# Optimization experiments

Measured on AMD Instinct MI355X. Metric: run time of the kernel, lower is better.

The kernel has to match this reference:

```python
import jax, jax.numpy as jnp
import numpy as np

DIM = 512
HEADS = 8
HEAD_DIM = DIM // HEADS // 2  # 32
KS = 7  # kernel_size
DIL = 1


def _window_and_pb_start(length, ks):
    nh = ks // 2
    i = jnp.arange(length)
    ni = jnp.clip(i - nh, 0, length - ks)                       # neighborhood start
    pi = nh + jnp.maximum(nh - i, 0) + jnp.where(i + nh >= length, length - i - 1 - nh, 0)
    return ni, pi


def na_attention(qkv_na, rpb):
    # qkv_na: [B,H,W,3*heads*hd]
    B, H, W, _ = qkv_na.shape
    qkv = qkv_na.reshape(B, H, W, 3, HEADS, HEAD_DIM)
    qkv = jnp.transpose(qkv, (3, 0, 4, 1, 2, 5))                 # [3,B,h,H,W,d]
    q, k, v = qkv[0], qkv[1], qkv[2]
    scale = HEAD_DIM ** -0.5
    ni, pi = _window_and_pb_start(H, KS)
    nj, pj = _window_and_pb_start(W, KS)
    off = jnp.arange(KS)
    idx_i = ni[:, None] + off[None, :]                           # [H,K]
    idx_j = nj[:, None] + off[None, :]                           # [W,K]
    # gather neighborhoods: [B,h,H,W,K,K,d]
    kn = k[:, :, idx_i[:, None, :, None], idx_j[None, :, None, :], :]
    vn = v[:, :, idx_i[:, None, :, None], idx_j[None, :, None, :], :]
    bias_i = pi[:, None] + off[None, :]                          # [H,K]
    bias_j = pj[:, None] + off[None, :]                          # [W,K]
    bias = rpb[:, bias_i[:, None, :, None], bias_j[None, :, None, :]]  # [h,H,W,K,K]
    attn = jnp.einsum('bhijd,bhijkld->bhijkl', q * scale, kn) + bias[None]
    a = attn.reshape(B, HEADS, H, W, KS * KS)
    a = jax.nn.softmax(a, axis=-1).reshape(B, HEADS, H, W, KS, KS)
    out = jnp.einsum('bhijkl,bhijkld->bhijd', a, vn)             # [B,h,H,W,d]
    return jnp.transpose(out, (0, 2, 3, 1, 4)).reshape(B, H, W, HEADS * HEAD_DIM)


def self_attention(qkv_self):
    # qkv_self: [B,H,W,3*heads*hd]
    B, H, W, _ = qkv_self.shape
    N = H * W
    qkv = qkv_self.reshape(B, N, 3, HEADS, HEAD_DIM)
    qkv = jnp.transpose(qkv, (2, 0, 3, 1, 4))                    # [3,B,h,N,d]
    q, k, v = qkv[0], qkv[1], qkv[2]
    scale = HEAD_DIM ** -0.5
    scores = jnp.einsum('bhnd,bhmd->bhnm', q * scale, k)
    a = jax.nn.softmax(scores, axis=-1)
    out = jnp.einsum('bhnm,bhmd->bhnd', a, v)
    out = jnp.transpose(out, (0, 2, 1, 3)).reshape(B, H, W, HEADS * HEAD_DIM)
    return out


def setup_inputs() -> dict:
    key = jax.random.key(0)
    ks = jax.random.split(key, 6)
    B, H, W = 2, 48, 48
    x = jax.random.normal(ks[0], (B, H, W, DIM), dtype=jnp.float32)
    W_qkv = jax.random.normal(ks[1], (DIM, 3 * DIM), dtype=jnp.float32) * (DIM ** -0.5)
    b_qkv = jax.random.normal(ks[2], (3 * DIM,), dtype=jnp.float32) * 0.02
    rpb = jax.random.normal(ks[3], (HEADS, 2 * KS - 1, 2 * KS - 1), dtype=jnp.float32) * 0.02
    W_proj = jax.random.normal(ks[4], (DIM, DIM), dtype=jnp.float32) * (DIM ** -0.5)
    b_proj = jax.random.normal(ks[5], (DIM,), dtype=jnp.float32) * 0.02
    return {"x": x, "W_qkv": W_qkv, "b_qkv": b_qkv, "rpb": rpb, "W_proj": W_proj, "b_proj": b_proj}


def reference(x, W_qkv, b_qkv, rpb, W_proj, b_proj):
    B, H, W, C = x.shape
    qkv = x @ W_qkv + b_qkv                                      # [B,H,W,3C]
    qkv_na, qkv_self = qkv[..., : 3 * C // 2], qkv[..., 3 * C // 2:]
    x_na = na_attention(qkv_na, rpb)                             # [B,H,W,C//2]
    x_self = self_attention(qkv_self)                            # [B,H,W,C//2]
    out = jnp.concatenate([x_na, x_self], axis=-1) @ W_proj + b_proj
    return out
```

## Files before the change

kernel.cpp:

```cpp
#include <hip/hip_runtime.h>
#include <cstdint>
#include <cstddef>


#define DIMC 512
#define HEADS 8
#define HD 32
#define KSZ 7
#define HH 48
#define WW 48
#define BB 2
#define NPIX (HH * WW)
#define ROWS (BB * NPIX)
#define C3 (3 * DIMC)
#define TK 64
#define KSPLIT 4
#define KCHUNK (NPIX / KSPLIT)
#define NTILES (KCHUNK / TK)
#define QB 128
#define NQBLK (NPIX / QB)
#define ROWE 40
#define VSTR 72
#define VROWE 232
#define LOG2E 1.4426950408889634f

typedef __attribute__((ext_vector_type(8))) short short8;
typedef __attribute__((ext_vector_type(4))) float f32x4;
union frag8 { short8 s; uint32_t u[4]; };

static __device__ __forceinline__ float bf2f(uint32_t u) {
    return __builtin_bit_cast(float, u << 16);
}
static __device__ __forceinline__ uint16_t f2bf(float f) {
    uint32_t x = __builtin_bit_cast(uint32_t, f);
    uint32_t r = x + 0x7fffu + ((x >> 16) & 1u);
    return (uint16_t)(r >> 16);
}
static __device__ __forceinline__ uint32_t cvtpk(float lo, float hi) {
    uint32_t r;
    asm("v_cvt_pk_bf16_f32 %0, %1, %2" : "=v"(r) : "v"(lo), "v"(hi));
    return r;
}
static __device__ __forceinline__ float ex2(float x) {
    return __builtin_amdgcn_exp2f(x);
}

__global__ __launch_bounds__(256)
void transpose_to_bf16(const float* __restrict__ W, uint16_t* __restrict__ Wt,
                       int K, int N)
{
    __shared__ float tile[32][33];
    const int tx = threadIdx.x & 31, ty = threadIdx.x >> 5;
    const int k0 = blockIdx.x * 32, n0 = blockIdx.y * 32;
    #pragma unroll
    for (int i = 0; i < 4; ++i)
        tile[ty + 8 * i][tx] = W[(size_t)(k0 + ty + 8 * i) * N + n0 + tx];
    __syncthreads();
    #pragma unroll
    for (int i = 0; i < 4; ++i)
        Wt[(size_t)(n0 + ty + 8 * i) * K + k0 + tx] = f2bf(tile[tx][ty + 8 * i]);
}

template<bool A_F32, bool OUT_F32, bool QSCALE>
__global__ __launch_bounds__(256)
void gemm_mfma(const void* __restrict__ Av, const uint16_t* __restrict__ Bt,
               const float* __restrict__ bias, void* __restrict__ Cv,
               int M, int N, int K)
{
    constexpr int BM = 128, BK = 32;
    constexpr float QSC = 0.17677669529663687f * LOG2E;
    __shared__ __align__(16) uint16_t Al[BM * ROWE];
    __shared__ __align__(16) uint16_t Bl[BM * ROWE];
    const int tid = threadIdx.x;
    const int lane = tid & 63, wv = tid >> 6;
    const int c = lane & 15, g = lane >> 4;
    const int wr = wv >> 1, wc = wv & 1;
    const int m0 = blockIdx.y * BM, n0 = blockIdx.x * BM;
    const int srow = tid >> 2, skc = (tid & 3) * 8;

    f32x4 acc[4][4];
    #pragma unroll
    for (int mi = 0; mi < 4; ++mi)
        #pragma unroll
        for (int ni = 0; ni < 4; ++ni)
            acc[mi][ni] = (f32x4){0.f, 0.f, 0.f, 0.f};

    for (int k0 = 0; k0 < K; k0 += BK) {
        __syncthreads();
        #pragma unroll
        for (int half = 0; half < 2; ++half) {
            const int row = srow + half * 64;
            if (A_F32) {
                const float* A32 = (const float*)Av;
                const float4 a0 = *reinterpret_cast<const float4*>(&A32[(size_t)(m0 + row) * K + k0 + skc]);
                const float4 a1 = *reinterpret_cast<const float4*>(&A32[(size_t)(m0 + row) * K + k0 + skc + 4]);
                *reinterpret_cast<uint4*>(&Al[row * ROWE + skc]) =
                    make_uint4(cvtpk(a0.x, a0.y), cvtpk(a0.z, a0.w),
                               cvtpk(a1.x, a1.y), cvtpk(a1.z, a1.w));
            } else {
                const uint16_t* A16 = (const uint16_t*)Av;
                *reinterpret_cast<uint4*>(&Al[row * ROWE + skc]) =
                    *reinterpret_cast<const uint4*>(&A16[(size_t)(m0 + row) * K + k0 + skc]);
            }
            *reinterpret_cast<uint4*>(&Bl[row * ROWE + skc]) =
                *reinterpret_cast<const uint4*>(&Bt[(size_t)(n0 + row) * K + k0 + skc]);
        }
        __syncthreads();

        frag8 a[4], b[4];
        #pragma unroll
        for (int mi = 0; mi < 4; ++mi)
            a[mi].s = *reinterpret_cast<const short8*>(&Al[(wr * 64 + mi * 16 + c) * ROWE + g * 8]);
        #pragma unroll
        for (int ni = 0; ni < 4; ++ni)
            b[ni].s = *reinterpret_cast<const short8*>(&Bl[(wc * 64 + ni * 16 + c) * ROWE + g * 8]);
        #pragma unroll
        for (int mi = 0; mi < 4; ++mi)
            #pragma unroll
            for (int ni = 0; ni < 4; ++ni)
                acc[mi][ni] = __builtin_amdgcn_mfma_f32_16x16x32_bf16(
                    a[mi].s, b[ni].s, acc[mi][ni], 0, 0, 0);
    }

    #pragma unroll
    for (int mi = 0; mi < 4; ++mi) {
        #pragma unroll
        for (int ni = 0; ni < 4; ++ni) {
            const int row = m0 + wr * 64 + mi * 16 + 4 * g;
            const int col = n0 + wc * 64 + ni * 16 + c;
            const float bv = bias[col];
            float f = 1.f;
            if (QSCALE) f = (col < 256 || (col >= 768 && col < 1024)) ? QSC : 1.f;
            #pragma unroll
            for (int r = 0; r < 4; ++r) {
                const float val = (acc[mi][ni][r] + bv) * f;
                if (OUT_F32)
                    ((float*)Cv)[(size_t)(row + r) * N + col] = val;
                else
                    ((uint16_t*)Cv)[(size_t)(row + r) * N + col] = f2bf(val);
            }
        }
    }
}

__global__ __launch_bounds__(256)
void na_attn_mfma(const uint16_t* __restrict__ qkv, const float* __restrict__ rpb,
                  uint16_t* __restrict__ attn)
{
    const int tid = threadIdx.x;
    const int lane = tid & 63, wv = tid >> 6;
    const int c = lane & 15, g = lane >> 4, g4 = g * 4;
    const int bid = blockIdx.x;
    const int tile = bid % 36;
    const int bh = bid / 36;
    const int h = bh & (HEADS - 1), b = bh >> 3;
    const int t0i = (tile / 6) * 8, t0j = (tile % 6) * 8;
    const int u0i = min(max(t0i - 3, 0), HH - 14);
    const int u0j = min(max(t0j - 3, 0), WW - 14);
    const size_t rowbase = (size_t)b * NPIX;

    __shared__ __align__(16) uint16_t K_l[224 * ROWE];
    __shared__ __align__(16) uint16_t Vt[32 * VROWE];
    __shared__ float rpb_l[169];

    if (tid < 169) rpb_l[tid] = rpb[h * 169 + tid] * LOG2E;
    #pragma unroll
    for (int it = 0; it < 4; ++it) {
        const int idx = it * 256 + tid;
        if (idx < 896) {
            const int u = idx >> 2, dc = idx & 3;
            const int uc = u & 15, ur = u >> 4;
            if (uc < 14) {
                const int grow = (u0i + ur) * WW + (u0j + uc);
                const uint16_t* src = qkv + (rowbase + grow) * C3 + 256 + h * HD + dc * 8;
                *reinterpret_cast<uint4*>(&K_l[u * ROWE + dc * 8]) =
                    *reinterpret_cast<const uint4*>(src);
                const uint4 vw = *reinterpret_cast<const uint4*>(src + 256);
                const uint16_t* vh = reinterpret_cast<const uint16_t*>(&vw);
                #pragma unroll
                for (int i = 0; i < 8; ++i)
                    Vt[(dc * 8 + i) * VROWE + u] = vh[i];
            } else {
                *reinterpret_cast<uint4*>(&K_l[u * ROWE + dc * 8]) = make_uint4(0, 0, 0, 0);
                #pragma unroll
                for (int i = 0; i < 8; ++i)
                    Vt[(dc * 8 + i) * VROWE + u] = 0;
            }
        }
    }

    const int qid = wv * 16 + c;
    const int qi = t0i + (qid >> 3), qj = t0j + (qid & 7);
    const int pixq = qi * WW + qj;
    const int niq = min(max(qi - 3, 0), HH - KSZ);
    const int njq = min(max(qj - 3, 0), WW - KSZ);
    const int piq = 3 + max(3 - qi, 0) + ((qi + 3 >= HH) ? (HH - qi - 4) : 0);
    const int pjq = 3 + max(3 - qj, 0) + ((qj + 3 >= WW) ? (WW - qj - 4) : 0);
    const int ni_rel = niq - u0i, nj_rel = njq - u0j;
    const int bb = (piq - ni_rel) * 13 + (pjq - nj_rel);

    frag8 qf;
    qf.s = *reinterpret_cast<const short8*>(qkv + (rowbase + pixq) * C3 + h * HD + g * 8);

    __syncthreads();

    float pex[14][4];
    float m = -1e30f;
    #pragma unroll
    for (int f = 0; f < 14; ++f) {
        frag8 ka;
        ka.s = *reinterpret_cast<const short8*>(&K_l[(16 * f + c) * ROWE + g * 8]);
        f32x4 s = {0.f, 0.f, 0.f, 0.f};
        s = __builtin_amdgcn_mfma_f32_16x16x32_bf16(ka.s, qf.s, s, 0, 0, 0);
        const bool rok = (unsigned)(f - ni_rel) < 7u;
        #pragma unroll
        for (int r = 0; r < 4; ++r) {
            const int uc = g4 + r;
            const bool ok = rok && ((unsigned)(uc - nj_rel) < 7u);
            const int addr = ok ? (bb + 13 * f + uc) : 0;
            const float v = s[r] + rpb_l[addr];
            pex[f][r] = ok ? v : -1e30f;
            m = fmaxf(m, pex[f][r]);
        }
    }
    m = fmaxf(m, __shfl_xor(m, 16));
    m = fmaxf(m, __shfl_xor(m, 32));
    float l = 0.f;
    #pragma unroll
    for (int f = 0; f < 14; ++f)
        #pragma unroll
        for (int r = 0; r < 4; ++r) {
            pex[f][r] = ex2(pex[f][r] - m);
            l += pex[f][r];
        }
    l += __shfl_xor(l, 16);
    l += __shfl_xor(l, 32);

    f32x4 of0 = {0.f, 0.f, 0.f, 0.f}, of1 = {0.f, 0.f, 0.f, 0.f};
    const int sbase = (g & 1) * 32 + c;
    #pragma unroll
    for (int kk = 0; kk < 7; ++kk) {
        uint32_t pk0[2], pk1[2];
        pk0[0] = cvtpk(pex[2 * kk][0], pex[2 * kk][1]);
        pk0[1] = cvtpk(pex[2 * kk][2], pex[2 * kk][3]);
        pk1[0] = cvtpk(pex[2 * kk + 1][0], pex[2 * kk + 1][1]);
        pk1[1] = cvtpk(pex[2 * kk + 1][2], pex[2 * kk + 1][3]);
        frag8 pb;
        #pragma unroll
        for (int tt = 0; tt < 4; ++tt) {
            const int srcLane = sbase + ((tt >> 1) << 4);
            const uint32_t v0 = __shfl(pk0[tt & 1], srcLane);
            const uint32_t v1 = __shfl(pk1[tt & 1], srcLane);
            pb.u[tt] = (g >= 2) ? v1 : v0;
        }
        frag8 va0, va1;
        va0.s = *reinterpret_cast<const short8*>(&Vt[c * VROWE + kk * 32 + g * 8]);
        va1.s = *reinterpret_cast<const short8*>(&Vt[(16 + c) * VROWE + kk * 32 + g * 8]);
        of0 = __builtin_amdgcn_mfma_f32_16x16x32_bf16(va0.s, pb.s, of0, 0, 0, 0);
        of1 = __builtin_amdgcn_mfma_f32_16x16x32_bf16(va1.s, pb.s, of1, 0, 0, 0);
    }

    const float invl = 1.f / l;
    uint32_t* dst = reinterpret_cast<uint32_t*>(attn + (rowbase + pixq) * DIMC + h * HD);
    dst[2 * g + 0] = cvtpk(of0[0] * invl, of0[1] * invl);
    dst[2 * g + 1] = cvtpk(of0[2] * invl, of0[3] * invl);
    dst[8 + 2 * g + 0] = cvtpk(of1[0] * invl, of1[1] * invl);
    dst[8 + 2 * g + 1] = cvtpk(of1[2] * invl, of1[3] * invl);
}

__global__ __launch_bounds__(256)
void self_attn_flash(const uint16_t* __restrict__ qkv,
                     uint16_t* __restrict__ po, float2* __restrict__ pml)
{
    const int tid = threadIdx.x;
    const int lane = tid & 63, wv = tid >> 6;
    const int c = lane & 15, g = lane >> 4;
    const int bid = blockIdx.x;
    const int split = bid & (KSPLIT - 1);
    const int qblk = (bid >> 2) % NQBLK;
    const int bh = bid / (KSPLIT * NQBLK);
    const int h = bh & (HEADS - 1);
    const int b = bh >> 3;
    const size_t rowbase = (size_t)b * NPIX;
    const int qbase = qblk * QB + wv * 32;
    const int q0 = qbase + c, q1 = qbase + 16 + c;

    __shared__ __align__(16) uint16_t Ks[2][TK * ROWE];
    __shared__ __align__(16) uint16_t Vt[2][32 * VSTR];

    frag8 qf0, qf1;
    qf0.s = *reinterpret_cast<const short8*>(qkv + (rowbase + q0) * C3 + 768 + h * HD + g * 8);
    qf1.s = *reinterpret_cast<const short8*>(qkv + (rowbase + q1) * C3 + 768 + h * HD + g * 8);

    float m0 = -1e30f, m1 = -1e30f, ls0 = 0.f, ls1 = 0.f;
    f32x4 oa00 = {0,0,0,0}, oa01 = {0,0,0,0};
    f32x4 oa10 = {0,0,0,0}, oa11 = {0,0,0,0};

    const int skk = tid >> 2, kd = (tid & 3) * 8;
    const int sgk = (skk & 15) | ((skk & 16) << 1) | ((skk & 32) >> 1);
    const int skv = tid >> 3, sdc = tid & 7;
    const int cp2 = 2 * (skv ^ ((sdc >> 1) << 3));

    uint4 KW; uint2 VA, VB;
#define STAGE_LOAD(T) do {                                                            \
    const size_t _tb = rowbase + split * KCHUNK + (T) * TK;                           \
    KW = *reinterpret_cast<const uint4*>(qkv + (_tb + sgk) * C3 + 1024 + h * HD + kd);\
    const uint16_t* _vp = qkv + (_tb + skv) * C3 + 1280 + h * HD + sdc * 4;           \
    VA = *reinterpret_cast<const uint2*>(_vp);                                        \
    VB = *reinterpret_cast<const uint2*>(_vp + 32 * C3); } while (0)

#define STAGE_WRITE(BUF) do {                                                         \
    *reinterpret_cast<uint4*>(&Ks[BUF][skk * ROWE + kd]) = KW;                        \
    const uint32_t _pa[4] = {VA.x & 0xffffu, VA.x >> 16, VA.y & 0xffffu, VA.y >> 16}; \
    const uint32_t _pb[4] = {VB.x & 0xffffu, VB.x >> 16, VB.y & 0xffffu, VB.y >> 16}; \
    _Pragma("unroll")                                                                 \
    for (int _i = 0; _i < 4; ++_i)                                                    \
        *reinterpret_cast<uint32_t*>(&Vt[BUF][(sdc * 4 + _i) * VSTR + cp2]) =         \
            _pa[_i] | (_pb[_i] << 16); } while (0)

    STAGE_LOAD(0);
    STAGE_WRITE(0);

    const int x0 = (c >> 3) << 3;
    const int x1 = 16 + x0;

    for (int t = 0; t < NTILES; ++t) {
        __syncthreads();

        const bool more = (t + 1 < NTILES);
        if (more) STAGE_LOAD(t + 1);

        const int cur = t & 1;
        frag8 ka0, ka1, ka2, ka3;
        ka0.s = *reinterpret_cast<const short8*>(&Ks[cur][c * ROWE + g * 8]);
        ka1.s = *reinterpret_cast<const short8*>(&Ks[cur][(16 + c) * ROWE + g * 8]);
        ka2.s = *reinterpret_cast<const short8*>(&Ks[cur][(32 + c) * ROWE + g * 8]);
        ka3.s = *reinterpret_cast<const short8*>(&Ks[cur][(48 + c) * ROWE + g * 8]);
        f32x4 sc0[4], sc1[4];
        #pragma unroll
        for (int kf = 0; kf < 4; ++kf) {
            sc0[kf] = (f32x4){0,0,0,0};
            sc1[kf] = (f32x4){0,0,0,0};
        }
        __builtin_amdgcn_s_setprio(1);
        sc0[0] = __builtin_amdgcn_mfma_f32_16x16x32_bf16(ka0.s, qf0.s, sc0[0], 0, 0, 0);
        sc0[1] = __builtin_amdgcn_mfma_f32_16x16x32_bf16(ka1.s, qf0.s, sc0[1], 0, 0, 0);
        sc0[2] = __builtin_amdgcn_mfma_f32_16x16x32_bf16(ka2.s, qf0.s, sc0[2], 0, 0, 0);
        sc0[3] = __builtin_amdgcn_mfma_f32_16x16x32_bf16(ka3.s, qf0.s, sc0[3], 0, 0, 0);
        sc1[0] = __builtin_amdgcn_mfma_f32_16x16x32_bf16(ka0.s, qf1.s, sc1[0], 0, 0, 0);
        sc1[1] = __builtin_amdgcn_mfma_f32_16x16x32_bf16(ka1.s, qf1.s, sc1[1], 0, 0, 0);
        sc1[2] = __builtin_amdgcn_mfma_f32_16x16x32_bf16(ka2.s, qf1.s, sc1[2], 0, 0, 0);
        sc1[3] = __builtin_amdgcn_mfma_f32_16x16x32_bf16(ka3.s, qf1.s, sc1[3], 0, 0, 0);
        __builtin_amdgcn_s_setprio(0);

        float t0 = sc0[0][0], t1 = sc1[0][0];
        #pragma unroll
        for (int kf = 0; kf < 4; ++kf)
            #pragma unroll
            for (int r = 0; r < 4; ++r) {
                t0 = fmaxf(t0, sc0[kf][r]);
                t1 = fmaxf(t1, sc1[kf][r]);
            }
        t0 = fmaxf(t0, __shfl_xor(t0, 16)); t0 = fmaxf(t0, __shfl_xor(t0, 32));
        t1 = fmaxf(t1, __shfl_xor(t1, 16)); t1 = fmaxf(t1, __shfl_xor(t1, 32));

        const int ok = (t0 - m0 <= 11.54f) && (t1 - m1 <= 11.54f);
        if (!__all(ok)) {
            const float nm0 = fmaxf(m0, t0), nm1 = fmaxf(m1, t1);
            const float c0 = ex2(m0 - nm0), c1 = ex2(m1 - nm1);
            ls0 *= c0; ls1 *= c1;
            oa00 *= c0; oa01 *= c0; oa10 *= c1; oa11 *= c1;
            m0 = nm0; m1 = nm1;
        }

        #pragma unroll
        for (int kf = 0; kf < 4; ++kf)
            #pragma unroll
            for (int r = 0; r < 4; ++r) {
                sc0[kf][r] = ex2(sc0[kf][r] - m0); ls0 += sc0[kf][r];
                sc1[kf][r] = ex2(sc1[kf][r] - m1); ls1 += sc1[kf][r];
            }

        #pragma unroll
        for (int kk = 0; kk < 2; ++kk) {
            frag8 pb0, pb1;
            #pragma unroll
            for (int tt = 0; tt < 4; ++tt) {
                pb0.u[tt] = cvtpk(sc0[2 * kk][tt], sc0[2 * kk + 1][tt]);
                pb1.u[tt] = cvtpk(sc1[2 * kk][tt], sc1[2 * kk + 1][tt]);
            }
            const int p0 = 16 * kk + 4 * g;
            frag8 va0, va1;
            va0.s = *reinterpret_cast<const short8*>(&Vt[cur][c * VSTR + 2 * (p0 ^ x0)]);
            va1.s = *reinterpret_cast<const short8*>(&Vt[cur][(16 + c) * VSTR + 2 * (p0 ^ x1)]);
            __builtin_amdgcn_s_setprio(1);
            oa00 = __builtin_amdgcn_mfma_f32_16x16x32_bf16(va0.s, pb0.s, oa00, 0, 0, 0);
            oa01 = __builtin_amdgcn_mfma_f32_16x16x32_bf16(va1.s, pb0.s, oa01, 0, 0, 0);
            oa10 = __builtin_amdgcn_mfma_f32_16x16x32_bf16(va0.s, pb1.s, oa10, 0, 0, 0);
            oa11 = __builtin_amdgcn_mfma_f32_16x16x32_bf16(va1.s, pb1.s, oa11, 0, 0, 0);
            __builtin_amdgcn_s_setprio(0);
        }

        if (more) STAGE_WRITE(cur ^ 1);
    }

    ls0 += __shfl_xor(ls0, 16); ls0 += __shfl_xor(ls0, 32);
    ls1 += __shfl_xor(ls1, 16); ls1 += __shfl_xor(ls1, 32);

    const float i0 = 1.f / ls0, i1 = 1.f / ls1;
    const size_t item0 = ((size_t)split * 16 + bh) * NPIX + q0;
    const size_t item1 = ((size_t)split * 16 + bh) * NPIX + q1;
    uint32_t* d0 = reinterpret_cast<uint32_t*>(po + item0 * HD);
    d0[2 * g + 0] = cvtpk(oa00[0] * i0, oa00[1] * i0);
    d0[2 * g + 1] = cvtpk(oa00[2] * i0, oa00[3] * i0);
    d0[8 + 2 * g + 0] = cvtpk(oa01[0] * i0, oa01[1] * i0);
    d0[8 + 2 * g + 1] = cvtpk(oa01[2] * i0, oa01[3] * i0);
    uint32_t* d1 = reinterpret_cast<uint32_t*>(po + item1 * HD);
    d1[2 * g + 0] = cvtpk(oa10[0] * i1, oa10[1] * i1);
    d1[2 * g + 1] = cvtpk(oa10[2] * i1, oa10[3] * i1);
    d1[8 + 2 * g + 0] = cvtpk(oa11[0] * i1, oa11[1] * i1);
    d1[8 + 2 * g + 1] = cvtpk(oa11[2] * i1, oa11[3] * i1);
    if (g == 0) {
        pml[item0] = make_float2(m0, ls0);
        pml[item1] = make_float2(m1, ls1);
    }
#undef STAGE_LOAD
#undef STAGE_WRITE
}

__global__ __launch_bounds__(256)
void self_attn_combine(const uint16_t* __restrict__ po, const float2* __restrict__ pml,
                       uint16_t* __restrict__ attn)
{
    const int idx = blockIdx.x * 256 + threadIdx.x;
    const int d = idx & (HD - 1);
    const int q = (idx >> 5) % NPIX;
    const int bh = idx / (HD * NPIX);
    const int h = bh & (HEADS - 1);
    const int b = bh >> 3;

    float2 ml[KSPLIT];
    float M = -1e30f;
    #pragma unroll
    for (int s = 0; s < KSPLIT; ++s) {
        ml[s] = pml[((size_t)s * 16 + bh) * NPIX + q];
        M = fmaxf(M, ml[s].x);
    }
    float num = 0.f, den = 0.f;
    #pragma unroll
    for (int s = 0; s < KSPLIT; ++s) {
        const float w = ex2(ml[s].x - M) * ml[s].y;
        const float o = bf2f((uint32_t)po[(((size_t)s * 16 + bh) * NPIX + q) * HD + d]);
        num = fmaf(w, o, num);
        den += w;
    }
    attn[((size_t)b * NPIX + q) * DIMC + 256 + h * HD + d] = f2bf(num / den);
}

extern "C" void kernel_launch(void* const* d_in, const int* in_sizes, int n_in,
                              void* d_out, int out_size, void* d_ws, size_t ws_size,
                              hipStream_t stream)
{
    const float* x     = (const float*)d_in[0];
    const float* Wqkv  = (const float*)d_in[1];
    const float* bqkv  = (const float*)d_in[2];
    const float* rpb   = (const float*)d_in[3];
    const float* Wproj = (const float*)d_in[4];
    const float* bproj = (const float*)d_in[5];

    uint16_t* qkv  = (uint16_t*)d_ws;
    uint16_t* attn = qkv + (size_t)ROWS * C3;
    uint16_t* wqt  = attn + (size_t)ROWS * DIMC;
    uint16_t* wpt  = wqt + (size_t)C3 * DIMC;
    float2*   pml  = (float2*)(wpt + (size_t)DIMC * DIMC);
    uint16_t* po   = (uint16_t*)d_out;

    const dim3 blk(256);
    transpose_to_bf16<<<dim3(DIMC / 32, C3 / 32), blk, 0, stream>>>(Wqkv, wqt, DIMC, C3);
    transpose_to_bf16<<<dim3(DIMC / 32, DIMC / 32), blk, 0, stream>>>(Wproj, wpt, DIMC, DIMC);
    gemm_mfma<true, false, true><<<dim3(C3 / 128, ROWS / 128), blk, 0, stream>>>(
        x, wqt, bqkv, qkv, ROWS, C3, DIMC);
    na_attn_mfma<<<dim3(BB * HEADS * 36), blk, 0, stream>>>(qkv, rpb, attn);
    self_attn_flash<<<dim3(16 * NQBLK * KSPLIT), blk, 0, stream>>>(qkv, po, pml);
    self_attn_combine<<<dim3((16 * NPIX * HD) / 256), blk, 0, stream>>>(po, pml, attn);
    gemm_mfma<false, true, false><<<dim3(DIMC / 128, ROWS / 128), blk, 0, stream>>>(
        attn, wpt, bproj, d_out, ROWS, DIMC, DIMC);
}
```

Baseline: 94.71 us.

## Fuse split-K self-attention combine into projection GEMM A-load and merge weight transposes

The separate split-K combine kernel is removed. The projection GEMM now rebuilds the self-attention half of its A operand on the fly from the partial outputs and max/sum pairs while staging A into LDS. The two weight-transpose launches are also merged into a single launch. This saves two kernel launches and one write and read of the combined attention buffer. In exchange, the combine work is repeated for each of the 4 N-tile column blocks of the GEMM, which adds redundant global reads and math to the GEMM's load path.

```diff
diff --git a/kernel.cpp b/kernel.cpp
--- a/kernel.cpp
+++ b/kernel.cpp
@@ -46,12 +46,18 @@
 }
 
 __global__ __launch_bounds__(256)
-void transpose_to_bf16(const float* __restrict__ W, uint16_t* __restrict__ Wt,
-                       int K, int N)
+void prep_weights(const float* __restrict__ Wqkv, const float* __restrict__ Wproj,
+                  uint16_t* __restrict__ wqt, uint16_t* __restrict__ wpt)
 {
     __shared__ float tile[32][33];
+    int bid = blockIdx.x;
+    const float* W; uint16_t* Wt; int N;
+    if (bid < 768) { W = Wqkv; Wt = wqt; N = C3; }
+    else { bid -= 768; W = Wproj; Wt = wpt; N = DIMC; }
+    const int kt = bid & 15, nt = bid >> 4;
+    const int K = DIMC;
     const int tx = threadIdx.x & 31, ty = threadIdx.x >> 5;
-    const int k0 = blockIdx.x * 32, n0 = blockIdx.y * 32;
+    const int k0 = kt * 32, n0 = nt * 32;
     #pragma unroll
     for (int i = 0; i < 4; ++i)
         tile[ty + 8 * i][tx] = W[(size_t)(k0 + ty + 8 * i) * N + n0 + tx];
@@ -61,11 +67,12 @@
         Wt[(size_t)(n0 + ty + 8 * i) * K + k0 + tx] = f2bf(tile[tx][ty + 8 * i]);
 }
 
-template<bool A_F32, bool OUT_F32, bool QSCALE>
+template<bool A_F32, bool OUT_F32, bool QSCALE, bool COMBINE>
 __global__ __launch_bounds__(256)
 void gemm_mfma(const void* __restrict__ Av, const uint16_t* __restrict__ Bt,
                const float* __restrict__ bias, void* __restrict__ Cv,
-               int M, int N, int K)
+               int M, int N, int K,
+               const uint16_t* __restrict__ po, const float2* __restrict__ pml)
 {
     constexpr int BM = 128, BK = 32;
     constexpr float QSC = 0.17677669529663687f * LOG2E;
@@ -90,7 +97,54 @@
         #pragma unroll
         for (int half = 0; half < 2; ++half) {
             const int row = srow + half * 64;
-            if (A_F32) {
+            if (COMBINE) {
+                const int col0 = k0 + skc;
+                const int rglob = m0 + row;
+                if (col0 < 256) {
+                    *reinterpret_cast<uint4*>(&Al[row * ROWE + skc]) =
+                        *reinterpret_cast<const uint4*>(
+                            &((const uint16_t*)Av)[(size_t)rglob * 256 + col0]);
+                } else {
+                    const int cs = col0 - 256;
+                    const int hh = cs >> 5, d0 = cs & 31;
+                    const int bb_ = (rglob >= NPIX) ? 1 : 0;
+                    const int q = rglob - bb_ * NPIX;
+                    const size_t base = (size_t)(bb_ * 8 + hh) * NPIX + q;
+                    float2 ml[KSPLIT];
+                    float M2 = -1e30f;
+                    #pragma unroll
+                    for (int s = 0; s < KSPLIT; ++s) {
+                        ml[s] = pml[(size_t)s * 16 * NPIX + base];
+                        M2 = fmaxf(M2, ml[s].x);
+                    }
+                    float w[KSPLIT], den = 0.f;
+                    #pragma unroll
+                    for (int s = 0; s < KSPLIT; ++s) {
+                        w[s] = ex2(ml[s].x - M2) * ml[s].y;
+                        den += w[s];
+                    }
+                    const float inv = 1.f / den;
+                    uint4 pv[KSPLIT];
+                    #pragma unroll
+                    for (int s = 0; s < KSPLIT; ++s)
+                        pv[s] = *reinterpret_cast<const uint4*>(
+                            &po[((size_t)s * 16 * NPIX + base) * HD + d0]);
+                    uint32_t outw[4];
+                    #pragma unroll
+                    for (int jp = 0; jp < 4; ++jp) {
+                        float nlo = 0.f, nhi = 0.f;
+                        #pragma unroll
+                        for (int s = 0; s < KSPLIT; ++s) {
+                            const uint32_t wd = (&pv[s].x)[jp];
+                            nlo = fmaf(w[s], bf2f(wd & 0xffffu), nlo);
+                            nhi = fmaf(w[s], bf2f(wd >> 16), nhi);
+                        }
+                        outw[jp] = cvtpk(nlo * inv, nhi * inv);
+                    }
+                    *reinterpret_cast<uint4*>(&Al[row * ROWE + skc]) =
+                        make_uint4(outw[0], outw[1], outw[2], outw[3]);
+                }
+            } else if (A_F32) {
                 const float* A32 = (const float*)Av;
                 const float4 a0 = *reinterpret_cast<const float4*>(&A32[(size_t)(m0 + row) * K + k0 + skc]);
                 const float4 a1 = *reinterpret_cast<const float4*>(&A32[(size_t)(m0 + row) * K + k0 + skc + 4]);
@@ -145,7 +199,7 @@
 
 __global__ __launch_bounds__(256)
 void na_attn_mfma(const uint16_t* __restrict__ qkv, const float* __restrict__ rpb,
-                  uint16_t* __restrict__ attn)
+                  uint16_t* __restrict__ attn_na)
 {
     const int tid = threadIdx.x;
     const int lane = tid & 63, wv = tid >> 6;
@@ -261,7 +315,7 @@
     }
 
     const float invl = 1.f / l;
-    uint32_t* dst = reinterpret_cast<uint32_t*>(attn + (rowbase + pixq) * DIMC + h * HD);
+    uint32_t* dst = reinterpret_cast<uint32_t*>(attn_na + (rowbase + pixq) * 256 + h * HD);
     dst[2 * g + 0] = cvtpk(of0[0] * invl, of0[1] * invl);
     dst[2 * g + 1] = cvtpk(of0[2] * invl, of0[3] * invl);
     dst[8 + 2 * g + 0] = cvtpk(of1[0] * invl, of1[1] * invl);
@@ -428,35 +482,6 @@
 #undef STAGE_WRITE
 }
 
-__global__ __launch_bounds__(256)
-void self_attn_combine(const uint16_t* __restrict__ po, const float2* __restrict__ pml,
-                       uint16_t* __restrict__ attn)
-{
-    const int idx = blockIdx.x * 256 + threadIdx.x;
-    const int d = idx & (HD - 1);
-    const int q = (idx >> 5) % NPIX;
-    const int bh = idx / (HD * NPIX);
-    const int h = bh & (HEADS - 1);
-    const int b = bh >> 3;
-
-    float2 ml[KSPLIT];
-    float M = -1e30f;
-    #pragma unroll
-    for (int s = 0; s < KSPLIT; ++s) {
-        ml[s] = pml[((size_t)s * 16 + bh) * NPIX + q];
-        M = fmaxf(M, ml[s].x);
-    }
-    float num = 0.f, den = 0.f;
-    #pragma unroll
-    for (int s = 0; s < KSPLIT; ++s) {
-        const float w = ex2(ml[s].x - M) * ml[s].y;
-        const float o = bf2f((uint32_t)po[(((size_t)s * 16 + bh) * NPIX + q) * HD + d]);
-        num = fmaf(w, o, num);
-        den += w;
-    }
-    attn[((size_t)b * NPIX + q) * DIMC + 256 + h * HD + d] = f2bf(num / den);
-}
-
 extern "C" void kernel_launch(void* const* d_in, const int* in_sizes, int n_in,
                               void* d_out, int out_size, void* d_ws, size_t ws_size,
                               hipStream_t stream)
@@ -468,21 +493,19 @@
     const float* Wproj = (const float*)d_in[4];
     const float* bproj = (const float*)d_in[5];
 
-    uint16_t* qkv  = (uint16_t*)d_ws;
-    uint16_t* attn = qkv + (size_t)ROWS * C3;
-    uint16_t* wqt  = attn + (size_t)ROWS * DIMC;
-    uint16_t* wpt  = wqt + (size_t)C3 * DIMC;
-    float2*   pml  = (float2*)(wpt + (size_t)DIMC * DIMC);
-    uint16_t* po   = (uint16_t*)d_out;
+    uint16_t* qkv     = (uint16_t*)d_ws;
+    uint16_t* attn_na = qkv + (size_t)ROWS * C3;
+    uint16_t* wqt     = attn_na + (size_t)ROWS * 256;
+    uint16_t* wpt     = wqt + (size_t)C3 * DIMC;
+    uint16_t* po      = wpt + (size_t)DIMC * DIMC;
+    float2*   pml     = (float2*)(po + (size_t)KSPLIT * 16 * NPIX * HD);
 
     const dim3 blk(256);
-    transpose_to_bf16<<<dim3(DIMC / 32, C3 / 32), blk, 0, stream>>>(Wqkv, wqt, DIMC, C3);
-    transpose_to_bf16<<<dim3(DIMC / 32, DIMC / 32), blk, 0, stream>>>(Wproj, wpt, DIMC, DIMC);
-    gemm_mfma<true, false, true><<<dim3(C3 / 128, ROWS / 128), blk, 0, stream>>>(
-        x, wqt, bqkv, qkv, ROWS, C3, DIMC);
-    na_attn_mfma<<<dim3(BB * HEADS * 36), blk, 0, stream>>>(qkv, rpb, attn);
+    prep_weights<<<dim3(1024), blk, 0, stream>>>(Wqkv, Wproj, wqt, wpt);
+    gemm_mfma<true, false, true, false><<<dim3(C3 / 128, ROWS / 128), blk, 0, stream>>>(
+        x, wqt, bqkv, qkv, ROWS, C3, DIMC, nullptr, nullptr);
+    na_attn_mfma<<<dim3(BB * HEADS * 36), blk, 0, stream>>>(qkv, rpb, attn_na);
     self_attn_flash<<<dim3(16 * NQBLK * KSPLIT), blk, 0, stream>>>(qkv, po, pml);
-    self_attn_combine<<<dim3((16 * NPIX * HD) / 256), blk, 0, stream>>>(po, pml, attn);
-    gemm_mfma<false, true, false><<<dim3(DIMC / 128, ROWS / 128), blk, 0, stream>>>(
-        attn, wpt, bproj, d_out, ROWS, DIMC, DIMC);
-}
+    gemm_mfma<false, true, false, true><<<dim3(DIMC / 128, ROWS / 128), blk, 0, stream>>>(
+        attn_na, wpt, bproj, d_out, ROWS, DIMC, DIMC, po, pml);
+}
```

Result: slower. 100.8 us (+6.4%).
